# Performance work log

Measured on AMD Instinct MI355X. Metric: run time of the kernel, lower is better.

The kernel has to match this reference:

```python
import jax, jax.numpy as jnp
import numpy as np

T, B, L = 40, 64, 80
D_IN = 256
H = 4 * D_IN  # 1024
A = 18


def _lstm_scan(x, h0, c0, W_ih, W_hh, b_ih, b_hh):
    # x: [S,B,in] -> outputs [S,B,H]; PyTorch gate order i,f,g,o
    b = b_ih + b_hh
    def step(carry, xt):
        h, c = carry
        g = xt @ W_ih.T + h @ W_hh.T + b
        i, f, gg, o = jnp.split(g, 4, axis=-1)
        c = jax.nn.sigmoid(f) * c + jax.nn.sigmoid(i) * jnp.tanh(gg)
        h = jax.nn.sigmoid(o) * jnp.tanh(c)
        return (h, c), h
    (h, c), ys = jax.lax.scan(step, (h0, c0), x)
    return ys, h, c


def setup_inputs() -> dict:
    key = jax.random.key(0)
    ks = jax.random.split(key, 24)
    def rn(k, shape, scale=0.02):
        return jax.random.normal(k, shape, dtype=jnp.float32) * scale
    return {
        "state": rn(ks[0], (T, B, D_IN), 1.0),
        "demonstration": rn(ks[1], (T, B, L, D_IN), 1.0),
        "demonstration_length": jax.random.randint(ks[2], (T, B), 1, L + 1, dtype=jnp.int32),
        "h0": jnp.zeros((B, H), jnp.float32),
        "c0": jnp.zeros((B, H), jnp.float32),
        "enc_Wih": rn(ks[3], (4 * H, D_IN)),
        "enc_Whh": rn(ks[4], (4 * H, H)),
        "enc_bih": rn(ks[5], (4 * H,)),
        "enc_bhh": rn(ks[6], (4 * H,)),
        "attn_W": rn(ks[7], (1, 2 * H)),
        "attn_b": rn(ks[8], (1,)),
        "comb_W": rn(ks[9], (H, H + D_IN)),
        "comb_b": rn(ks[10], (H,)),
        "lstm_Wih": rn(ks[11], (4 * H, H)),
        "lstm_Whh": rn(ks[12], (4 * H, H)),
        "lstm_bih": rn(ks[13], (4 * H,)),
        "lstm_bhh": rn(ks[14], (4 * H,)),
        "mid_W": rn(ks[15], (H, H)),
        "mid_b": rn(ks[16], (H,)),
        "out_W": rn(ks[17], (A, H)),
        "out_b": rn(ks[18], (A,)),
    }


def reference(state, demonstration, demonstration_length, h0, c0,
              enc_Wih, enc_Whh, enc_bih, enc_bhh,
              attn_W, attn_b, comb_W, comb_b,
              lstm_Wih, lstm_Whh, lstm_bih, lstm_bhh,
              mid_W, mid_b, out_W, out_b):
    lengths = demonstration_length[0]              # [B], only t=0 lengths used (as in original)
    demo0 = demonstration[0]                       # [B,L,D_IN], only t=0 demo used
    z = jnp.zeros((B, H), demo0.dtype)
    enc, _, _ = _lstm_scan(demo0.transpose(1, 0, 2), z, z,
                           enc_Wih, enc_Whh, enc_bih, enc_bhh)  # [L,B,H]
    enc = enc.transpose(1, 0, 2)                   # [B,L,H]
    mask = jnp.arange(L)[None, :] < lengths[:, None]  # [B,L]
    # attn(cat(enc, h)) == enc @ Wd^T + h @ Wh^T + b (split of the concat linear)
    Wd, Wh = attn_W[:, :H], attn_W[:, H:]          # [1,H] each
    score_d = (enc @ Wd.T)[..., 0] + attn_b[0]     # [B,L], constant over t
    lstm_b = lstm_bih + lstm_bhh

    def step(carry, obs_t):
        h, c = carry
        scores = score_d + h @ Wh.T                # [B,L] ([B,1] broadcast)
        scores = jnp.where(mask, scores, -jnp.inf)
        w = jax.nn.softmax(scores, axis=-1)        # masked softmax over demo steps
        attn_applied = jnp.einsum('bl,blh->bh', w, enc)
        x = jax.nn.relu(jnp.concatenate([attn_applied, obs_t], axis=-1) @ comb_W.T + comb_b)
        g = x @ lstm_Wih.T + h @ lstm_Whh.T + lstm_b
        i, f, gg, o = jnp.split(g, 4, axis=-1)
        c = jax.nn.sigmoid(f) * c + jax.nn.sigmoid(i) * jnp.tanh(gg)
        h = jax.nn.sigmoid(o) * jnp.tanh(c)
        m = h @ mid_W.T + mid_b                    # no activation between middle and output (as in source)
        q_t = m @ out_W.T + out_b
        return (h, c), q_t

    (h, c), q = jax.lax.scan(step, (h0, c0), state)  # q: [T,B,A]
    return q, h, c
```

## Files before the change

kernel.cpp:

```cpp
#include <hip/hip_runtime.h>
#include <hip/hip_bf16.h>

#define TT 40
#define BB 64
#define LL 80
#define DD 256
#define HH 1024
#define G4H 4096
#define AA 18
#define KENC 1280
#define KLSTM 2048
#define KCOMB 1280
#define NB 256
#define NT 512
#define QSZ (TT*BB*AA)

typedef __bf16 bf16x8 __attribute__((ext_vector_type(8)));
typedef float  f32x4  __attribute__((ext_vector_type(4)));

#define OFF_WENC   ((size_t)0)
#define OFF_WLSTM  (OFF_WENC  + (size_t)G4H*KENC*2)
#define OFF_WCOMB  (OFF_WLSTM + (size_t)G4H*KLSTM*2)
#define OFF_WMID   (OFF_WCOMB + (size_t)HH*KCOMB*2)
#define OFF_BIASE  (OFF_WMID  + (size_t)HH*HH*2)
#define OFF_BIASL  (OFF_BIASE + (size_t)G4H*4)
#define OFF_DEMO   (OFF_BIASL + (size_t)G4H*4)
#define OFF_STATE  (OFF_DEMO  + (size_t)BB*LL*DD*2)
#define OFF_ENC    (OFF_STATE + (size_t)TT*BB*DD*2)
#define OFF_HDEC   (OFF_ENC   + (size_t)BB*LL*HH*2)
#define OFF_XALL   (OFF_HDEC  + (size_t)TT*BB*HH*2)
#define OFF_MF     (OFF_XALL  + (size_t)TT*BB*HH*2)
#define OFF_ATTNS  (OFF_MF    + (size_t)TT*BB*HH*2)
#define OFF_HROT   (OFF_ATTNS + (size_t)BB*HH*2)
#define NSLOT_E    81
#define NSLOT_D    41
#define OFF_BAR    (OFF_HROT  + (size_t)(NSLOT_E+NSLOT_D)*BB*HH*2)
#define FLAG_STRIDE 16
#define BAR_BYTES  (NB*FLAG_STRIDE*4)

__device__ __forceinline__ float sigm(float x){ return 1.f/(1.f+__expf(-x)); }

__device__ __forceinline__ float wred_sum(float v){
#pragma unroll
  for (int s=32; s>0; s>>=1) v += __shfl_xor(v, s, 64);
  return v;
}
__device__ __forceinline__ float wred_max(float v){
#pragma unroll
  for (int s=32; s>0; s>>=1) v = fmaxf(v, __shfl_xor(v, s, 64));
  return v;
}

__device__ __forceinline__ unsigned pack_bf16(float a, float b){
  unsigned short ua = __builtin_bit_cast(unsigned short, (__bf16)a);
  unsigned short ub = __builtin_bit_cast(unsigned short, (__bf16)b);
  return (unsigned)ua | ((unsigned)ub << 16);
}

__device__ __forceinline__ void st_u32_sc(unsigned* p, unsigned v){
  __hip_atomic_store(p, v, __ATOMIC_RELAXED, __HIP_MEMORY_SCOPE_AGENT);
}
__device__ __forceinline__ void st_b16_sc(__bf16* p, float v){
  unsigned short u = __builtin_bit_cast(unsigned short, (__bf16)v);
  asm volatile("global_store_short %0, %1, off sc0 sc1"
               :: "v"(p), "v"((unsigned)u) : "memory");
}

__device__ __forceinline__ void gbar_arrive(unsigned* flags, unsigned target, int bk){
  __syncthreads();
  if (threadIdx.x == 0) {
    __builtin_amdgcn_fence(__ATOMIC_RELEASE, "agent");
    __hip_atomic_store(flags + (size_t)bk*FLAG_STRIDE, target,
                       __ATOMIC_RELAXED, __HIP_MEMORY_SCOPE_AGENT);
  }
}
__device__ __forceinline__ void gbar_wait(unsigned* flags, unsigned target){
  if (threadIdx.x < 64) {
    unsigned long long spins = 0;
    for (;;) {
      unsigned a0 = __hip_atomic_load(flags + (size_t)threadIdx.x*FLAG_STRIDE,       __ATOMIC_RELAXED, __HIP_MEMORY_SCOPE_AGENT);
      unsigned a1 = __hip_atomic_load(flags + (size_t)(64+threadIdx.x)*FLAG_STRIDE,  __ATOMIC_RELAXED, __HIP_MEMORY_SCOPE_AGENT);
      unsigned a2 = __hip_atomic_load(flags + (size_t)(128+threadIdx.x)*FLAG_STRIDE, __ATOMIC_RELAXED, __HIP_MEMORY_SCOPE_AGENT);
      unsigned a3 = __hip_atomic_load(flags + (size_t)(192+threadIdx.x)*FLAG_STRIDE, __ATOMIC_RELAXED, __HIP_MEMORY_SCOPE_AGENT);
      bool ok = (a0 >= target) && (a1 >= target) && (a2 >= target) && (a3 >= target);
      if (__all((int)ok)) break;
      if (++spins > (1ull<<20)) break;
      __builtin_amdgcn_s_sleep(1);
    }
  }
  __syncthreads();
  asm volatile("" ::: "memory");
}

__global__ void k_pack_enc(const float* __restrict__ wih, const float* __restrict__ whh,
                           const float* __restrict__ bih, const float* __restrict__ bhh,
                           __bf16* __restrict__ dst, float* __restrict__ bias){
  int p = blockIdx.x;
  int gate = p & 3, jj = (p >> 2) & 3, bq = p >> 4;
  int orig = gate*HH + bq*4 + jj;
  if (threadIdx.x == 0) bias[p] = bih[orig] + bhh[orig];
  const float* s0 = wih + (size_t)orig*DD;
  const float* s1 = whh + (size_t)orig*HH;
  __bf16* d = dst + (size_t)p*KENC;
  for (int k = threadIdx.x; k < KENC; k += blockDim.x)
    d[k] = (__bf16)(k < DD ? s0[k] : s1[k-DD]);
}
__global__ void k_pack_lstm(const float* __restrict__ wih, const float* __restrict__ whh,
                            const float* __restrict__ bih, const float* __restrict__ bhh,
                            __bf16* __restrict__ dst, float* __restrict__ bias){
  int p = blockIdx.x;
  int gate = p & 3, jj = (p >> 2) & 3, bq = p >> 4;
  int orig = gate*HH + bq*4 + jj;
  if (threadIdx.x == 0) bias[p] = bih[orig] + bhh[orig];
  const float* s0 = wih + (size_t)orig*HH;
  const float* s1 = whh + (size_t)orig*HH;
  __bf16* d = dst + (size_t)p*KLSTM;
  for (int k = threadIdx.x; k < KLSTM; k += blockDim.x)
    d[k] = (__bf16)(k < HH ? s0[k] : s1[k-HH]);
}
__global__ void k_conv(const float* __restrict__ src, __bf16* __restrict__ dst, int n){
  int i = blockIdx.x*blockDim.x + threadIdx.x;
  if (i < n) dst[i] = (__bf16)src[i];
}

__global__ __launch_bounds__(NT, 1)
void k_main(const int* __restrict__ demlen,
            const float* __restrict__ h0, const float* __restrict__ c0,
            const float* __restrict__ attn_w,
            const float* __restrict__ comb_b, const float* __restrict__ mid_b,
            const float* __restrict__ out_w, const float* __restrict__ out_b,
            float* __restrict__ out, char* __restrict__ ws){
  const int bk = blockIdx.x, tid = threadIdx.x;
  const int wv = tid >> 6, ln = tid & 63;
  const int l15 = ln & 15, lhi = ln >> 4;
  const int klane = lhi * 8;
  const int gtid = bk*NT + tid;

  __bf16* wEnc  = (__bf16*)(ws + OFF_WENC);
  __bf16* wLstm = (__bf16*)(ws + OFF_WLSTM);
  __bf16* wComb = (__bf16*)(ws + OFF_WCOMB);
  __bf16* wMid  = (__bf16*)(ws + OFF_WMID);
  const float* bE = (const float*)(ws + OFF_BIASE);
  const float* bL = (const float*)(ws + OFF_BIASL);
  __bf16* demoC = (__bf16*)(ws + OFF_DEMO);
  __bf16* stateB= (__bf16*)(ws + OFF_STATE);
  __bf16* encB  = (__bf16*)(ws + OFF_ENC);
  __bf16* hdec  = (__bf16*)(ws + OFF_HDEC);
  __bf16* xall  = (__bf16*)(ws + OFF_XALL);
  __bf16* mf    = (__bf16*)(ws + OFF_MF);
  __bf16* attnS = (__bf16*)(ws + OFF_ATTNS);
  __bf16* hrotE = (__bf16*)(ws + OFF_HROT);
  __bf16* hrotD = hrotE + (size_t)NSLOT_E*BB*HH;
  unsigned* flags = (unsigned*)(ws + OFF_BAR);

  __shared__ float g_lds [BB*17];
  __shared__ float g_lds2[BB*17];
  __shared__ float sc_sh[LL];
  __shared__ float w_sh[LL];

  unsigned bar = 0;
  const int m_ = tid >> 1, q2 = tid & 1;
  const int j0_ = bk*4 + 2*q2;
  const int mt = wv & 3;
  const int am = mt*16 + l15;
  const int khalf = wv >> 2;

  float cfa = 0.f, cfb = 0.f;

  for (int i = gtid; i < BB*HH/2; i += NB*NT) st_u32_sc((unsigned*)hrotE + i, 0u);
  ++bar; gbar_arrive(flags, bar, bk);

  for (int t = 0; t < LL; ++t) {
    gbar_wait(flags, bar);
    const __bf16* hR = hrotE + (size_t)t*BB*HH;
    const __bf16* brow = wEnc + (size_t)(bk*16 + l15)*KENC;
    const int kbase = khalf * 640;

    f32x4 acc = {0.f,0.f,0.f,0.f};
#pragma unroll 8
    for (int kk = 0; kk < 640; kk += 32) {
      int k0 = kbase + kk + klane;
      const __bf16* pa = (k0 < DD) ? demoC + ((size_t)am*LL + t)*DD + k0
                                   : hR + (size_t)am*HH + (k0 - DD);
      acc = __builtin_amdgcn_mfma_f32_16x16x32_bf16(*(const bf16x8*)pa,
                                                    *(const bf16x8*)(brow + k0), acc, 0,0,0);
    }
    {
      float* gl = khalf ? g_lds2 : g_lds;
      int r0 = mt*16 + lhi*4;
#pragma unroll
      for (int r = 0; r < 4; ++r) gl[(r0+r)*17 + l15] = acc[r];
    }
    __syncthreads();
    if (tid < 128) {
      char* hWg = (char*)(hrotE + (size_t)(t+1)*BB*HH);
      int gb = m_*17 + q2*8, cb = bk*16 + q2*8;
      float gi0 = g_lds[gb+0]+g_lds2[gb+0]+bE[cb+0], gf0 = g_lds[gb+1]+g_lds2[gb+1]+bE[cb+1];
      float gg0 = g_lds[gb+2]+g_lds2[gb+2]+bE[cb+2], go0 = g_lds[gb+3]+g_lds2[gb+3]+bE[cb+3];
      float gi1 = g_lds[gb+4]+g_lds2[gb+4]+bE[cb+4], gf1 = g_lds[gb+5]+g_lds2[gb+5]+bE[cb+5];
      float gg1 = g_lds[gb+6]+g_lds2[gb+6]+bE[cb+6], go1 = g_lds[gb+7]+g_lds2[gb+7]+bE[cb+7];
      float cn0 = sigm(gf0)*cfa + sigm(gi0)*tanhf(gg0);
      float cn1 = sigm(gf1)*cfb + sigm(gi1)*tanhf(gg1);
      float hn0 = sigm(go0)*tanhf(cn0);
      float hn1 = sigm(go1)*tanhf(cn1);
      cfa = cn0; cfb = cn1;
      unsigned hp = pack_bf16(hn0, hn1);
      st_u32_sc((unsigned*)(hWg + m_*2048 + j0_*2), hp);
      st_u32_sc((unsigned*)(encB + ((size_t)m_*LL + t)*HH + j0_), hp);
    }
    ++bar; gbar_arrive(flags, bar, bk);
  }

  gbar_wait(flags, bar);
  {
    int b = bk >> 2, qq = bk & 3;
    for (int i = 0; i < 10; ++i) {
      int l = wv*10 + i;
      const __bf16* er = encB + ((size_t)b*LL + l)*HH + ln*16;
      bf16x8 e0 = *(const bf16x8*)(er);
      bf16x8 e1 = *(const bf16x8*)(er + 8);
      float part = 0.f;
#pragma unroll
      for (int j = 0; j < 8; ++j) {
        part += (float)e0[j] * attn_w[ln*16 + j];
        part += (float)e1[j] * attn_w[ln*16 + 8 + j];
      }
      part = wred_sum(part);
      if (ln == 0) sc_sh[l] = part;
    }
    __syncthreads();
    if (wv == 0) {
      int len = demlen[b];
      float s0 = (ln < len) ? sc_sh[ln] : -1e30f;
      float s1 = (ln < 16 && 64+ln < len) ? sc_sh[64+ln] : -1e30f;
      float mx = wred_max(fmaxf(s0, s1));
      float e0 = __expf(s0 - mx);
      float e1 = (ln < 16) ? __expf(s1 - mx) : 0.f;
      float inv = 1.f / wred_sum(e0 + e1);
      w_sh[ln] = e0 * inv;
      if (ln < 16) w_sh[64+ln] = e1 * inv;
    }
    __syncthreads();
    if (tid < 256) {
      int col = qq*256 + tid;
      float a = 0.f;
      const __bf16* eb = encB + (size_t)b*LL*HH + col;
#pragma unroll 4
      for (int l = 0; l < LL; ++l) a += w_sh[l] * (float)eb[(size_t)l*HH];
      st_b16_sc(attnS + (size_t)b*HH + col, a);
    }
    for (int i = gtid; i < BB*HH/2; i += NB*NT) {
      int i2 = i*2;
      st_u32_sc((unsigned*)hrotD + i, pack_bf16(h0[i2], h0[i2+1]));
    }
    if (tid < 128) {
      cfa = c0[m_*HH + j0_];
      cfb = c0[m_*HH + j0_ + 1];
    }
  }
  ++bar; gbar_arrive(flags, bar, bk);

  gbar_wait(flags, bar);
  {
    int g = bk*8 + wv;
    for (int i = 0; i < 5; ++i) {
      int ti = i*2048 + g;
      int mtt = ti >> 6, nt = ti & 63;
      f32x4 acc = {0.f,0.f,0.f,0.f};
      const __bf16* brow = wComb + (size_t)(nt*16 + l15)*KCOMB;
      int r = mtt*16 + l15, bb = r & 63;
      const __bf16* aat = attnS + (size_t)bb*HH;
      const __bf16* ast = stateB + (size_t)r*DD;
#pragma unroll 8
      for (int kk = 0; kk < KCOMB; kk += 32) {
        int k0 = kk + klane;
        bf16x8 af = (k0 < HH) ? *(const bf16x8*)(aat + k0)
                              : *(const bf16x8*)(ast + (k0-HH));
        acc = __builtin_amdgcn_mfma_f32_16x16x32_bf16(af, *(const bf16x8*)(brow + k0), acc, 0,0,0);
      }
      int col = nt*16 + l15;
      float cb = comb_b[col];
      int r0 = mtt*16 + lhi*4;
#pragma unroll
      for (int rr = 0; rr < 4; ++rr)
        st_b16_sc(xall + (size_t)(r0+rr)*HH + col, fmaxf(acc[rr]+cb, 0.f));
    }
  }
  ++bar; gbar_arrive(flags, bar, bk);

  for (int t = 0; t < TT; ++t) {
    gbar_wait(flags, bar);
    const __bf16* hR = hrotD + (size_t)t*BB*HH;
    const __bf16* brow = wLstm + (size_t)(bk*16 + l15)*KLSTM;
    const int kbase = khalf * HH;
    const __bf16* arow = khalf ? (hR + (size_t)am*HH)
                               : (xall + ((size_t)t*BB + am)*HH);

    f32x4 acc = {0.f,0.f,0.f,0.f};
#pragma unroll 8
    for (int kk = 0; kk < HH; kk += 32) {
      int k0 = kk + klane;
      acc = __builtin_amdgcn_mfma_f32_16x16x32_bf16(*(const bf16x8*)(arow + k0),
                                                    *(const bf16x8*)(brow + kbase + k0), acc, 0,0,0);
    }
    {
      float* gl = khalf ? g_lds2 : g_lds;
      int r0 = mt*16 + lhi*4;
#pragma unroll
      for (int r = 0; r < 4; ++r) gl[(r0+r)*17 + l15] = acc[r];
    }
    __syncthreads();
    if (tid < 128) {
      char* hWg = (char*)(hrotD + (size_t)(t+1)*BB*HH);
      int gb = m_*17 + q2*8, cb = bk*16 + q2*8;
      float gi0 = g_lds[gb+0]+g_lds2[gb+0]+bL[cb+0], gf0 = g_lds[gb+1]+g_lds2[gb+1]+bL[cb+1];
      float gg0 = g_lds[gb+2]+g_lds2[gb+2]+bL[cb+2], go0 = g_lds[gb+3]+g_lds2[gb+3]+bL[cb+3];
      float gi1 = g_lds[gb+4]+g_lds2[gb+4]+bL[cb+4], gf1 = g_lds[gb+5]+g_lds2[gb+5]+bL[cb+5];
      float gg1 = g_lds[gb+6]+g_lds2[gb+6]+bL[cb+6], go1 = g_lds[gb+7]+g_lds2[gb+7]+bL[cb+7];
      float cn0 = sigm(gf0)*cfa + sigm(gi0)*tanhf(gg0);
      float cn1 = sigm(gf1)*cfb + sigm(gi1)*tanhf(gg1);
      float hn0 = sigm(go0)*tanhf(cn0);
      float hn1 = sigm(go1)*tanhf(cn1);
      cfa = cn0; cfb = cn1;
      unsigned hp = pack_bf16(hn0, hn1);
      st_u32_sc((unsigned*)(hWg + m_*2048 + j0_*2), hp);
      st_u32_sc((unsigned*)(hdec + ((size_t)t*BB + m_)*HH + j0_), hp);
      if (t == TT-1) {
        out[QSZ + m_*HH + j0_]     = hn0;
        out[QSZ + m_*HH + j0_ + 1] = hn1;
      }
    }
    ++bar; gbar_arrive(flags, bar, bk);
  }

  if (tid < 128) {
    out[QSZ + BB*HH + m_*HH + j0_]     = cfa;
    out[QSZ + BB*HH + m_*HH + j0_ + 1] = cfb;
  }

  gbar_wait(flags, bar);
  {
    int g = bk*8 + wv;
    for (int i = 0; i < 5; ++i) {
      int ti = i*2048 + g;
      int mtt = ti >> 6, nt = ti & 63;
      f32x4 acc = {0.f,0.f,0.f,0.f};
      const __bf16* brow = wMid + (size_t)(nt*16 + l15)*HH;
      const __bf16* arow2 = hdec + (size_t)(mtt*16 + l15)*HH;
#pragma unroll 8
      for (int kk = 0; kk < HH; kk += 32) {
        int k0 = kk + klane;
        acc = __builtin_amdgcn_mfma_f32_16x16x32_bf16(*(const bf16x8*)(arow2 + k0),
                                                      *(const bf16x8*)(brow + k0), acc, 0,0,0);
      }
      int col = nt*16 + l15;
      float mb = mid_b[col];
      int r0 = mtt*16 + lhi*4;
#pragma unroll
      for (int rr = 0; rr < 4; ++rr)
        st_b16_sc(mf + (size_t)(r0+rr)*HH + col, acc[rr]+mb);
    }
  }
  ++bar; gbar_arrive(flags, bar, bk);

  gbar_wait(flags, bar);
  {
    int g = bk*8 + wv;
    for (int i = 0; i < 2; ++i) {
      int row = i*2048 + g;
      if (row < TT*BB) {
        const __bf16* mr = mf + (size_t)row*HH;
        float mreg[16];
#pragma unroll
        for (int k = 0; k < 16; ++k) mreg[k] = (float)mr[ln + 64*k];
        for (int a = 0; a < AA; ++a) {
          float p = 0.f;
#pragma unroll
          for (int k = 0; k < 16; ++k) p += mreg[k] * out_w[(size_t)a*HH + ln + 64*k];
          p = wred_sum(p);
          if (ln == 0) out[(size_t)row*AA + a] = p + out_b[a];
        }
      }
    }
  }
}

extern "C" void kernel_launch(void* const* d_in, const int* in_sizes, int n_in,
                              void* d_out, int out_size, void* d_ws, size_t ws_size,
                              hipStream_t stream) {
  (void)in_sizes; (void)n_in; (void)out_size; (void)ws_size;
  const float* state    = (const float*)d_in[0];
  const float* demo     = (const float*)d_in[1];
  const int*   demlen   = (const int*)d_in[2];
  const float* h0       = (const float*)d_in[3];
  const float* c0       = (const float*)d_in[4];
  const float* enc_wih  = (const float*)d_in[5];
  const float* enc_whh  = (const float*)d_in[6];
  const float* enc_bih  = (const float*)d_in[7];
  const float* enc_bhh  = (const float*)d_in[8];
  const float* attn_w   = (const float*)d_in[9];
  const float* comb_w   = (const float*)d_in[11];
  const float* comb_b   = (const float*)d_in[12];
  const float* lstm_wih = (const float*)d_in[13];
  const float* lstm_whh = (const float*)d_in[14];
  const float* lstm_bih = (const float*)d_in[15];
  const float* lstm_bhh = (const float*)d_in[16];
  const float* mid_w    = (const float*)d_in[17];
  const float* mid_b    = (const float*)d_in[18];
  const float* out_w    = (const float*)d_in[19];
  const float* out_b    = (const float*)d_in[20];
  char* ws = (char*)d_ws;

  (void)hipMemsetAsync(ws + OFF_BAR, 0, BAR_BYTES, stream);
  k_pack_enc <<<G4H, 256, 0, stream>>>(enc_wih, enc_whh, enc_bih, enc_bhh,
                                       (__bf16*)(ws + OFF_WENC), (float*)(ws + OFF_BIASE));
  k_pack_lstm<<<G4H, 256, 0, stream>>>(lstm_wih, lstm_whh, lstm_bih, lstm_bhh,
                                       (__bf16*)(ws + OFF_WLSTM), (float*)(ws + OFF_BIASL));
  k_conv<<<(HH*KCOMB + 255)/256, 256, 0, stream>>>(comb_w, (__bf16*)(ws + OFF_WCOMB), HH*KCOMB);
  k_conv<<<(HH*HH   + 255)/256, 256, 0, stream>>>(mid_w,  (__bf16*)(ws + OFF_WMID),  HH*HH);
  k_conv<<<(BB*LL*DD + 255)/256, 256, 0, stream>>>(demo,  (__bf16*)(ws + OFF_DEMO),  BB*LL*DD);
  k_conv<<<(TT*BB*DD + 255)/256, 256, 0, stream>>>(state, (__bf16*)(ws + OFF_STATE), TT*BB*DD);
  k_main<<<NB, NT, 0, stream>>>(demlen, h0, c0, attn_w, comb_b, mid_b,
                                out_w, out_b, (float*)d_out, ws);
}
```

Before: 2.125 ms.

## Replace persistent grid-barrier kernel with per-timestep kernel launches

Splits the single persistent kernel, which synchronised 256 blocks through spin-wait flag barriers, into separate launches: one per encoder step, one per decoder step, plus attention, combine, mid and output kernels. The h state ping-pongs between two buffers and the cell state lives in a global buffer instead of registers. This removes the cost of the software grid barrier and its sc0/sc1 coherent stores, but adds about 125 kernel launches with their launch latency and gaps.

```diff
diff --git a/kernel.cpp b/kernel.cpp
--- a/kernel.cpp
+++ b/kernel.cpp
@@ -11,8 +11,6 @@
 #define KENC 1280
 #define KLSTM 2048
 #define KCOMB 1280
-#define NB 256
-#define NT 512
 #define QSZ (TT*BB*AA)
 
 typedef __bf16 bf16x8 __attribute__((ext_vector_type(8)));
@@ -31,12 +29,8 @@
 #define OFF_XALL   (OFF_HDEC  + (size_t)TT*BB*HH*2)
 #define OFF_MF     (OFF_XALL  + (size_t)TT*BB*HH*2)
 #define OFF_ATTNS  (OFF_MF    + (size_t)TT*BB*HH*2)
-#define OFF_HROT   (OFF_ATTNS + (size_t)BB*HH*2)
-#define NSLOT_E    81
-#define NSLOT_D    41
-#define OFF_BAR    (OFF_HROT  + (size_t)(NSLOT_E+NSLOT_D)*BB*HH*2)
-#define FLAG_STRIDE 16
-#define BAR_BYTES  (NB*FLAG_STRIDE*4)
+#define OFF_CF     (OFF_ATTNS + (size_t)BB*HH*2)
+#define OFF_HBUF   (OFF_CF    + (size_t)BB*HH*4)
 
 __device__ __forceinline__ float sigm(float x){ return 1.f/(1.f+__expf(-x)); }
 
@@ -50,46 +44,10 @@
   for (int s=32; s>0; s>>=1) v = fmaxf(v, __shfl_xor(v, s, 64));
   return v;
 }
-
 __device__ __forceinline__ unsigned pack_bf16(float a, float b){
   unsigned short ua = __builtin_bit_cast(unsigned short, (__bf16)a);
   unsigned short ub = __builtin_bit_cast(unsigned short, (__bf16)b);
   return (unsigned)ua | ((unsigned)ub << 16);
-}
-
-__device__ __forceinline__ void st_u32_sc(unsigned* p, unsigned v){
-  __hip_atomic_store(p, v, __ATOMIC_RELAXED, __HIP_MEMORY_SCOPE_AGENT);
-}
-__device__ __forceinline__ void st_b16_sc(__bf16* p, float v){
-  unsigned short u = __builtin_bit_cast(unsigned short, (__bf16)v);
-  asm volatile("global_store_short %0, %1, off sc0 sc1"
-               :: "v"(p), "v"((unsigned)u) : "memory");
-}
-
-__device__ __forceinline__ void gbar_arrive(unsigned* flags, unsigned target, int bk){
-  __syncthreads();
-  if (threadIdx.x == 0) {
-    __builtin_amdgcn_fence(__ATOMIC_RELEASE, "agent");
-    __hip_atomic_store(flags + (size_t)bk*FLAG_STRIDE, target,
-                       __ATOMIC_RELAXED, __HIP_MEMORY_SCOPE_AGENT);
-  }
-}
-__device__ __forceinline__ void gbar_wait(unsigned* flags, unsigned target){
-  if (threadIdx.x < 64) {
-    unsigned long long spins = 0;
-    for (;;) {
-      unsigned a0 = __hip_atomic_load(flags + (size_t)threadIdx.x*FLAG_STRIDE,       __ATOMIC_RELAXED, __HIP_MEMORY_SCOPE_AGENT);
-      unsigned a1 = __hip_atomic_load(flags + (size_t)(64+threadIdx.x)*FLAG_STRIDE,  __ATOMIC_RELAXED, __HIP_MEMORY_SCOPE_AGENT);
-      unsigned a2 = __hip_atomic_load(flags + (size_t)(128+threadIdx.x)*FLAG_STRIDE, __ATOMIC_RELAXED, __HIP_MEMORY_SCOPE_AGENT);
-      unsigned a3 = __hip_atomic_load(flags + (size_t)(192+threadIdx.x)*FLAG_STRIDE, __ATOMIC_RELAXED, __HIP_MEMORY_SCOPE_AGENT);
-      bool ok = (a0 >= target) && (a1 >= target) && (a2 >= target) && (a3 >= target);
-      if (__all((int)ok)) break;
-      if (++spins > (1ull<<20)) break;
-      __builtin_amdgcn_s_sleep(1);
-    }
-  }
-  __syncthreads();
-  asm volatile("" ::: "memory");
 }
 
 __global__ void k_pack_enc(const float* __restrict__ wih, const float* __restrict__ whh,
@@ -123,266 +81,257 @@
   if (i < n) dst[i] = (__bf16)src[i];
 }
 
-__global__ __launch_bounds__(NT, 1)
-void k_main(const int* __restrict__ demlen,
-            const float* __restrict__ h0, const float* __restrict__ c0,
-            const float* __restrict__ attn_w,
-            const float* __restrict__ comb_b, const float* __restrict__ mid_b,
-            const float* __restrict__ out_w, const float* __restrict__ out_b,
-            float* __restrict__ out, char* __restrict__ ws){
+__global__ __launch_bounds__(256)
+void k_enc_step(const __bf16* __restrict__ demoC, const __bf16* __restrict__ wEnc,
+                const float* __restrict__ bE, const __bf16* __restrict__ hR,
+                __bf16* __restrict__ hW, __bf16* __restrict__ encB,
+                float* __restrict__ cf, int t){
   const int bk = blockIdx.x, tid = threadIdx.x;
   const int wv = tid >> 6, ln = tid & 63;
   const int l15 = ln & 15, lhi = ln >> 4;
   const int klane = lhi * 8;
-  const int gtid = bk*NT + tid;
-
-  __bf16* wEnc  = (__bf16*)(ws + OFF_WENC);
-  __bf16* wLstm = (__bf16*)(ws + OFF_WLSTM);
-  __bf16* wComb = (__bf16*)(ws + OFF_WCOMB);
-  __bf16* wMid  = (__bf16*)(ws + OFF_WMID);
-  const float* bE = (const float*)(ws + OFF_BIASE);
-  const float* bL = (const float*)(ws + OFF_BIASL);
-  __bf16* demoC = (__bf16*)(ws + OFF_DEMO);
-  __bf16* stateB= (__bf16*)(ws + OFF_STATE);
-  __bf16* encB  = (__bf16*)(ws + OFF_ENC);
-  __bf16* hdec  = (__bf16*)(ws + OFF_HDEC);
-  __bf16* xall  = (__bf16*)(ws + OFF_XALL);
-  __bf16* mf    = (__bf16*)(ws + OFF_MF);
-  __bf16* attnS = (__bf16*)(ws + OFF_ATTNS);
-  __bf16* hrotE = (__bf16*)(ws + OFF_HROT);
-  __bf16* hrotD = hrotE + (size_t)NSLOT_E*BB*HH;
-  unsigned* flags = (unsigned*)(ws + OFF_BAR);
-
-  __shared__ float g_lds [BB*17];
-  __shared__ float g_lds2[BB*17];
-  __shared__ float sc_sh[LL];
-  __shared__ float w_sh[LL];
-
-  unsigned bar = 0;
-  const int m_ = tid >> 1, q2 = tid & 1;
-  const int j0_ = bk*4 + 2*q2;
+  const int am = wv*16 + l15;
+
+  __shared__ float g_lds[BB*17];
+
+  const __bf16* brow = wEnc + (size_t)(bk*16 + l15)*KENC;
+  const __bf16* arow = demoC + ((size_t)am*LL + t)*DD;
+  const __bf16* hrow = hR + (size_t)am*HH;
+
+  f32x4 acc = {0.f,0.f,0.f,0.f};
+#pragma unroll 8
+  for (int kk = 0; kk < KENC; kk += 32) {
+    int k0 = kk + klane;
+    const __bf16* pa = (k0 < DD) ? (arow + k0) : (hrow + (k0 - DD));
+    acc = __builtin_amdgcn_mfma_f32_16x16x32_bf16(*(const bf16x8*)pa,
+                                                  *(const bf16x8*)(brow + k0), acc, 0,0,0);
+  }
+  {
+    int r0 = wv*16 + lhi*4;
+#pragma unroll
+    for (int r = 0; r < 4; ++r) g_lds[(r0+r)*17 + l15] = acc[r];
+  }
+  __syncthreads();
+  if (tid < 128) {
+    const int m_ = tid >> 1, q2 = tid & 1;
+    const int j0_ = bk*4 + 2*q2;
+    int gb = m_*17 + q2*8, cb = bk*16 + q2*8;
+    float gi0 = g_lds[gb+0]+bE[cb+0], gf0 = g_lds[gb+1]+bE[cb+1];
+    float gg0 = g_lds[gb+2]+bE[cb+2], go0 = g_lds[gb+3]+bE[cb+3];
+    float gi1 = g_lds[gb+4]+bE[cb+4], gf1 = g_lds[gb+5]+bE[cb+5];
+    float gg1 = g_lds[gb+6]+bE[cb+6], go1 = g_lds[gb+7]+bE[cb+7];
+    float cA = cf[m_*HH + j0_], cB = cf[m_*HH + j0_ + 1];
+    float cn0 = sigm(gf0)*cA + sigm(gi0)*tanhf(gg0);
+    float cn1 = sigm(gf1)*cB + sigm(gi1)*tanhf(gg1);
+    float hn0 = sigm(go0)*tanhf(cn0);
+    float hn1 = sigm(go1)*tanhf(cn1);
+    cf[m_*HH + j0_] = cn0; cf[m_*HH + j0_ + 1] = cn1;
+    unsigned hp = pack_bf16(hn0, hn1);
+    *(unsigned*)(hW + (size_t)m_*HH + j0_) = hp;
+    *(unsigned*)(encB + ((size_t)m_*LL + t)*HH + j0_) = hp;
+  }
+}
+
+__global__ __launch_bounds__(512)
+void k_dec_step(const __bf16* __restrict__ xall, const __bf16* __restrict__ wLstm,
+                const float* __restrict__ bL, const __bf16* __restrict__ hR,
+                __bf16* __restrict__ hW, __bf16* __restrict__ hdec,
+                float* __restrict__ cf, float* __restrict__ out, int t){
+  const int bk = blockIdx.x, tid = threadIdx.x;
+  const int wv = tid >> 6, ln = tid & 63;
+  const int l15 = ln & 15, lhi = ln >> 4;
+  const int klane = lhi * 8;
   const int mt = wv & 3;
   const int am = mt*16 + l15;
   const int khalf = wv >> 2;
 
-  float cfa = 0.f, cfb = 0.f;
-
-  for (int i = gtid; i < BB*HH/2; i += NB*NT) st_u32_sc((unsigned*)hrotE + i, 0u);
-  ++bar; gbar_arrive(flags, bar, bk);
-
-  for (int t = 0; t < LL; ++t) {
-    gbar_wait(flags, bar);
-    const __bf16* hR = hrotE + (size_t)t*BB*HH;
-    const __bf16* brow = wEnc + (size_t)(bk*16 + l15)*KENC;
-    const int kbase = khalf * 640;
-
+  __shared__ float g_lds [BB*17];
+  __shared__ float g_lds2[BB*17];
+
+  const __bf16* brow = wLstm + (size_t)(bk*16 + l15)*KLSTM + khalf*HH;
+  const __bf16* arow = khalf ? (hR + (size_t)am*HH)
+                             : (xall + ((size_t)t*BB + am)*HH);
+
+  f32x4 acc = {0.f,0.f,0.f,0.f};
+#pragma unroll 8
+  for (int kk = 0; kk < HH; kk += 32) {
+    int k0 = kk + klane;
+    acc = __builtin_amdgcn_mfma_f32_16x16x32_bf16(*(const bf16x8*)(arow + k0),
+                                                  *(const bf16x8*)(brow + k0), acc, 0,0,0);
+  }
+  {
+    float* gl = khalf ? g_lds2 : g_lds;
+    int r0 = mt*16 + lhi*4;
+#pragma unroll
+    for (int r = 0; r < 4; ++r) gl[(r0+r)*17 + l15] = acc[r];
+  }
+  __syncthreads();
+  if (tid < 128) {
+    const int m_ = tid >> 1, q2 = tid & 1;
+    const int j0_ = bk*4 + 2*q2;
+    int gb = m_*17 + q2*8, cb = bk*16 + q2*8;
+    float gi0 = g_lds[gb+0]+g_lds2[gb+0]+bL[cb+0], gf0 = g_lds[gb+1]+g_lds2[gb+1]+bL[cb+1];
+    float gg0 = g_lds[gb+2]+g_lds2[gb+2]+bL[cb+2], go0 = g_lds[gb+3]+g_lds2[gb+3]+bL[cb+3];
+    float gi1 = g_lds[gb+4]+g_lds2[gb+4]+bL[cb+4], gf1 = g_lds[gb+5]+g_lds2[gb+5]+bL[cb+5];
+    float gg1 = g_lds[gb+6]+g_lds2[gb+6]+bL[cb+6], go1 = g_lds[gb+7]+g_lds2[gb+7]+bL[cb+7];
+    float cA = cf[m_*HH + j0_], cB = cf[m_*HH + j0_ + 1];
+    float cn0 = sigm(gf0)*cA + sigm(gi0)*tanhf(gg0);
+    float cn1 = sigm(gf1)*cB + sigm(gi1)*tanhf(gg1);
+    float hn0 = sigm(go0)*tanhf(cn0);
+    float hn1 = sigm(go1)*tanhf(cn1);
+    cf[m_*HH + j0_] = cn0; cf[m_*HH + j0_ + 1] = cn1;
+    unsigned hp = pack_bf16(hn0, hn1);
+    *(unsigned*)(hW + (size_t)m_*HH + j0_) = hp;
+    *(unsigned*)(hdec + ((size_t)t*BB + m_)*HH + j0_) = hp;
+    if (t == TT-1) {
+      out[QSZ + m_*HH + j0_]     = hn0;
+      out[QSZ + m_*HH + j0_ + 1] = hn1;
+    }
+  }
+}
+
+__global__ __launch_bounds__(256)
+void k_attn(const int* __restrict__ demlen, const float* __restrict__ h0,
+            const float* __restrict__ c0, const float* __restrict__ attn_w,
+            const __bf16* __restrict__ encB, __bf16* __restrict__ attnS,
+            __bf16* __restrict__ hD0, float* __restrict__ cf){
+  const int bk = blockIdx.x, tid = threadIdx.x;
+  const int wv = tid >> 6, ln = tid & 63;
+  __shared__ float sc_sh[LL];
+  __shared__ float w_sh[LL];
+  int b = bk >> 2, qq = bk & 3;
+  for (int i = 0; i < 20; ++i) {
+    int l = wv*20 + i;
+    const __bf16* er = encB + ((size_t)b*LL + l)*HH + ln*16;
+    bf16x8 e0 = *(const bf16x8*)(er);
+    bf16x8 e1 = *(const bf16x8*)(er + 8);
+    float part = 0.f;
+#pragma unroll
+    for (int j = 0; j < 8; ++j) {
+      part += (float)e0[j] * attn_w[ln*16 + j];
+      part += (float)e1[j] * attn_w[ln*16 + 8 + j];
+    }
+    part = wred_sum(part);
+    if (ln == 0) sc_sh[l] = part;
+  }
+  __syncthreads();
+  if (wv == 0) {
+    int len = demlen[b];
+    float s0 = (ln < len) ? sc_sh[ln] : -1e30f;
+    float s1 = (ln < 16 && 64+ln < len) ? sc_sh[64+ln] : -1e30f;
+    float mx = wred_max(fmaxf(s0, s1));
+    float e0 = __expf(s0 - mx);
+    float e1 = (ln < 16) ? __expf(s1 - mx) : 0.f;
+    float inv = 1.f / wred_sum(e0 + e1);
+    w_sh[ln] = e0 * inv;
+    if (ln < 16) w_sh[64+ln] = e1 * inv;
+  }
+  __syncthreads();
+  {
+    int col = qq*256 + tid;
+    float a = 0.f;
+    const __bf16* eb = encB + (size_t)b*LL*HH + col;
+#pragma unroll 4
+    for (int l = 0; l < LL; ++l) a += w_sh[l] * (float)eb[(size_t)l*HH];
+    attnS[(size_t)b*HH + col] = (__bf16)a;
+  }
+  int gtid = bk*256 + tid;
+  for (int i = gtid; i < BB*HH/2; i += 256*256) {
+    int i2 = i*2;
+    *((unsigned*)hD0 + i) = pack_bf16(h0[i2], h0[i2+1]);
+  }
+  for (int i = gtid; i < BB*HH; i += 256*256) cf[i] = c0[i];
+}
+
+__global__ __launch_bounds__(256)
+void k_x(const __bf16* __restrict__ attnS, const __bf16* __restrict__ stateB,
+         const __bf16* __restrict__ wComb, const float* __restrict__ comb_b,
+         __bf16* __restrict__ xall){
+  const int bk = blockIdx.x, tid = threadIdx.x;
+  const int wv = tid >> 6, ln = tid & 63;
+  const int l15 = ln & 15, lhi = ln >> 4;
+  const int klane = lhi * 8;
+  int g = bk*4 + wv;
+  for (int i = 0; i < 10; ++i) {
+    int ti = i*1024 + g;
+    int mtt = ti >> 6, nt = ti & 63;
     f32x4 acc = {0.f,0.f,0.f,0.f};
+    const __bf16* brow = wComb + (size_t)(nt*16 + l15)*KCOMB;
+    int r = mtt*16 + l15, bb = r & 63;
+    const __bf16* aat = attnS + (size_t)bb*HH;
+    const __bf16* ast = stateB + (size_t)r*DD;
 #pragma unroll 8
-    for (int kk = 0; kk < 640; kk += 32) {
-      int k0 = kbase + kk + klane;
-      const __bf16* pa = (k0 < DD) ? demoC + ((size_t)am*LL + t)*DD + k0
-                                   : hR + (size_t)am*HH + (k0 - DD);
-      acc = __builtin_amdgcn_mfma_f32_16x16x32_bf16(*(const bf16x8*)pa,
-                                                    *(const bf16x8*)(brow + k0), acc, 0,0,0);
+    for (int kk = 0; kk < KCOMB; kk += 32) {
+      int k0 = kk + klane;
+      bf16x8 af = (k0 < HH) ? *(const bf16x8*)(aat + k0)
+                            : *(const bf16x8*)(ast + (k0-HH));
+      acc = __builtin_amdgcn_mfma_f32_16x16x32_bf16(af, *(const bf16x8*)(brow + k0), acc, 0,0,0);
     }
-    {
-      float* gl = khalf ? g_lds2 : g_lds;
-      int r0 = mt*16 + lhi*4;
-#pragma unroll
-      for (int r = 0; r < 4; ++r) gl[(r0+r)*17 + l15] = acc[r];
-    }
-    __syncthreads();
-    if (tid < 128) {
-      char* hWg = (char*)(hrotE + (size_t)(t+1)*BB*HH);
-      int gb = m_*17 + q2*8, cb = bk*16 + q2*8;
-      float gi0 = g_lds[gb+0]+g_lds2[gb+0]+bE[cb+0], gf0 = g_lds[gb+1]+g_lds2[gb+1]+bE[cb+1];
-      float gg0 = g_lds[gb+2]+g_lds2[gb+2]+bE[cb+2], go0 = g_lds[gb+3]+g_lds2[gb+3]+bE[cb+3];
-      float gi1 = g_lds[gb+4]+g_lds2[gb+4]+bE[cb+4], gf1 = g_lds[gb+5]+g_lds2[gb+5]+bE[cb+5];
-      float gg1 = g_lds[gb+6]+g_lds2[gb+6]+bE[cb+6], go1 = g_lds[gb+7]+g_lds2[gb+7]+bE[cb+7];
-      float cn0 = sigm(gf0)*cfa + sigm(gi0)*tanhf(gg0);
-      float cn1 = sigm(gf1)*cfb + sigm(gi1)*tanhf(gg1);
-      float hn0 = sigm(go0)*tanhf(cn0);
-      float hn1 = sigm(go1)*tanhf(cn1);
-      cfa = cn0; cfb = cn1;
-      unsigned hp = pack_bf16(hn0, hn1);
-      st_u32_sc((unsigned*)(hWg + m_*2048 + j0_*2), hp);
-      st_u32_sc((unsigned*)(encB + ((size_t)m_*LL + t)*HH + j0_), hp);
-    }
-    ++bar; gbar_arrive(flags, bar, bk);
-  }
-
-  gbar_wait(flags, bar);
-  {
-    int b = bk >> 2, qq = bk & 3;
-    for (int i = 0; i < 10; ++i) {
-      int l = wv*10 + i;
-      const __bf16* er = encB + ((size_t)b*LL + l)*HH + ln*16;
-      bf16x8 e0 = *(const bf16x8*)(er);
-      bf16x8 e1 = *(const bf16x8*)(er + 8);
-      float part = 0.f;
-#pragma unroll
-      for (int j = 0; j < 8; ++j) {
-        part += (float)e0[j] * attn_w[ln*16 + j];
-        part += (float)e1[j] * attn_w[ln*16 + 8 + j];
-      }
-      part = wred_sum(part);
-      if (ln == 0) sc_sh[l] = part;
-    }
-    __syncthreads();
-    if (wv == 0) {
-      int len = demlen[b];
-      float s0 = (ln < len) ? sc_sh[ln] : -1e30f;
-      float s1 = (ln < 16 && 64+ln < len) ? sc_sh[64+ln] : -1e30f;
-      float mx = wred_max(fmaxf(s0, s1));
-      float e0 = __expf(s0 - mx);
-      float e1 = (ln < 16) ? __expf(s1 - mx) : 0.f;
-      float inv = 1.f / wred_sum(e0 + e1);
-      w_sh[ln] = e0 * inv;
-      if (ln < 16) w_sh[64+ln] = e1 * inv;
-    }
-    __syncthreads();
-    if (tid < 256) {
-      int col = qq*256 + tid;
-      float a = 0.f;
-      const __bf16* eb = encB + (size_t)b*LL*HH + col;
-#pragma unroll 4
-      for (int l = 0; l < LL; ++l) a += w_sh[l] * (float)eb[(size_t)l*HH];
-      st_b16_sc(attnS + (size_t)b*HH + col, a);
-    }
-    for (int i = gtid; i < BB*HH/2; i += NB*NT) {
-      int i2 = i*2;
-      st_u32_sc((unsigned*)hrotD + i, pack_bf16(h0[i2], h0[i2+1]));
-    }
-    if (tid < 128) {
-      cfa = c0[m_*HH + j0_];
-      cfb = c0[m_*HH + j0_ + 1];
-    }
-  }
-  ++bar; gbar_arrive(flags, bar, bk);
-
-  gbar_wait(flags, bar);
-  {
-    int g = bk*8 + wv;
-    for (int i = 0; i < 5; ++i) {
-      int ti = i*2048 + g;
-      int mtt = ti >> 6, nt = ti & 63;
-      f32x4 acc = {0.f,0.f,0.f,0.f};
-      const __bf16* brow = wComb + (size_t)(nt*16 + l15)*KCOMB;
-      int r = mtt*16 + l15, bb = r & 63;
-      const __bf16* aat = attnS + (size_t)bb*HH;
-      const __bf16* ast = stateB + (size_t)r*DD;
-#pragma unroll 8
-      for (int kk = 0; kk < KCOMB; kk += 32) {
-        int k0 = kk + klane;
-        bf16x8 af = (k0 < HH) ? *(const bf16x8*)(aat + k0)
-                              : *(const bf16x8*)(ast + (k0-HH));
-        acc = __builtin_amdgcn_mfma_f32_16x16x32_bf16(af, *(const bf16x8*)(brow + k0), acc, 0,0,0);
-      }
-      int col = nt*16 + l15;
-      float cb = comb_b[col];
-      int r0 = mtt*16 + lhi*4;
-#pragma unroll
-      for (int rr = 0; rr < 4; ++rr)
-        st_b16_sc(xall + (size_t)(r0+rr)*HH + col, fmaxf(acc[rr]+cb, 0.f));
-    }
-  }
-  ++bar; gbar_arrive(flags, bar, bk);
-
-  for (int t = 0; t < TT; ++t) {
-    gbar_wait(flags, bar);
-    const __bf16* hR = hrotD + (size_t)t*BB*HH;
-    const __bf16* brow = wLstm + (size_t)(bk*16 + l15)*KLSTM;
-    const int kbase = khalf * HH;
-    const __bf16* arow = khalf ? (hR + (size_t)am*HH)
-                               : (xall + ((size_t)t*BB + am)*HH);
-
+    int col = nt*16 + l15;
+    float cb = comb_b[col];
+    int r0 = mtt*16 + lhi*4;
+#pragma unroll
+    for (int rr = 0; rr < 4; ++rr)
+      xall[(size_t)(r0+rr)*HH + col] = (__bf16)fmaxf(acc[rr]+cb, 0.f);
+  }
+}
+
+__global__ __launch_bounds__(256)
+void k_mid(const __bf16* __restrict__ hdec, const __bf16* __restrict__ wMid,
+           const float* __restrict__ mid_b, __bf16* __restrict__ mf){
+  const int bk = blockIdx.x, tid = threadIdx.x;
+  const int wv = tid >> 6, ln = tid & 63;
+  const int l15 = ln & 15, lhi = ln >> 4;
+  const int klane = lhi * 8;
+  int g = bk*4 + wv;
+  for (int i = 0; i < 10; ++i) {
+    int ti = i*1024 + g;
+    int mtt = ti >> 6, nt = ti & 63;
     f32x4 acc = {0.f,0.f,0.f,0.f};
+    const __bf16* brow = wMid + (size_t)(nt*16 + l15)*HH;
+    const __bf16* arow = hdec + (size_t)(mtt*16 + l15)*HH;
 #pragma unroll 8
     for (int kk = 0; kk < HH; kk += 32) {
       int k0 = kk + klane;
       acc = __builtin_amdgcn_mfma_f32_16x16x32_bf16(*(const bf16x8*)(arow + k0),
-                                                    *(const bf16x8*)(brow + kbase + k0), acc, 0,0,0);
+                                                    *(const bf16x8*)(brow + k0), acc, 0,0,0);
     }
-    {
-      float* gl = khalf ? g_lds2 : g_lds;
-      int r0 = mt*16 + lhi*4;
-#pragma unroll
-      for (int r = 0; r < 4; ++r) gl[(r0+r)*17 + l15] = acc[r];
-    }
-    __syncthreads();
-    if (tid < 128) {
-      char* hWg = (char*)(hrotD + (size_t)(t+1)*BB*HH);
-      int gb = m_*17 + q2*8, cb = bk*16 + q2*8;
-      float gi0 = g_lds[gb+0]+g_lds2[gb+0]+bL[cb+0], gf0 = g_lds[gb+1]+g_lds2[gb+1]+bL[cb+1];
-      float gg0 = g_lds[gb+2]+g_lds2[gb+2]+bL[cb+2], go0 = g_lds[gb+3]+g_lds2[gb+3]+bL[cb+3];
-      float gi1 = g_lds[gb+4]+g_lds2[gb+4]+bL[cb+4], gf1 = g_lds[gb+5]+g_lds2[gb+5]+bL[cb+5];
-      float gg1 = g_lds[gb+6]+g_lds2[gb+6]+bL[cb+6], go1 = g_lds[gb+7]+g_lds2[gb+7]+bL[cb+7];
-      float cn0 = sigm(gf0)*cfa + sigm(gi0)*tanhf(gg0);
-      float cn1 = sigm(gf1)*cfb + sigm(gi1)*tanhf(gg1);
-      float hn0 = sigm(go0)*tanhf(cn0);
-      float hn1 = sigm(go1)*tanhf(cn1);
-      cfa = cn0; cfb = cn1;
-      unsigned hp = pack_bf16(hn0, hn1);
-      st_u32_sc((unsigned*)(hWg + m_*2048 + j0_*2), hp);
-      st_u32_sc((unsigned*)(hdec + ((size_t)t*BB + m_)*HH + j0_), hp);
-      if (t == TT-1) {
-        out[QSZ + m_*HH + j0_]     = hn0;
-        out[QSZ + m_*HH + j0_ + 1] = hn1;
+    int col = nt*16 + l15;
+    float mb = mid_b[col];
+    int r0 = mtt*16 + lhi*4;
+#pragma unroll
+    for (int rr = 0; rr < 4; ++rr)
+      mf[(size_t)(r0+rr)*HH + col] = (__bf16)(acc[rr]+mb);
+  }
+}
+
+__global__ __launch_bounds__(256)
+void k_out(const __bf16* __restrict__ mf, const float* __restrict__ out_w,
+           const float* __restrict__ out_b, float* __restrict__ out){
+  const int bk = blockIdx.x, tid = threadIdx.x;
+  const int wv = tid >> 6, ln = tid & 63;
+  int g = bk*4 + wv;
+  for (int i = 0; i < 3; ++i) {
+    int row = i*1024 + g;
+    if (row < TT*BB) {
+      const __bf16* mr = mf + (size_t)row*HH;
+      float mreg[16];
+#pragma unroll
+      for (int k = 0; k < 16; ++k) mreg[k] = (float)mr[ln + 64*k];
+      for (int a = 0; a < AA; ++a) {
+        float p = 0.f;
+#pragma unroll
+        for (int k = 0; k < 16; ++k) p += mreg[k] * out_w[(size_t)a*HH + ln + 64*k];
+        p = wred_sum(p);
+        if (ln == 0) out[(size_t)row*AA + a] = p + out_b[a];
       }
     }
-    ++bar; gbar_arrive(flags, bar, bk);
-  }
-
-  if (tid < 128) {
-    out[QSZ + BB*HH + m_*HH + j0_]     = cfa;
-    out[QSZ + BB*HH + m_*HH + j0_ + 1] = cfb;
-  }
-
-  gbar_wait(flags, bar);
-  {
-    int g = bk*8 + wv;
-    for (int i = 0; i < 5; ++i) {
-      int ti = i*2048 + g;
-      int mtt = ti >> 6, nt = ti & 63;
-      f32x4 acc = {0.f,0.f,0.f,0.f};
-      const __bf16* brow = wMid + (size_t)(nt*16 + l15)*HH;
-      const __bf16* arow2 = hdec + (size_t)(mtt*16 + l15)*HH;
-#pragma unroll 8
-      for (int kk = 0; kk < HH; kk += 32) {
-        int k0 = kk + klane;
-        acc = __builtin_amdgcn_mfma_f32_16x16x32_bf16(*(const bf16x8*)(arow2 + k0),
-                                                      *(const bf16x8*)(brow + k0), acc, 0,0,0);
-      }
-      int col = nt*16 + l15;
-      float mb = mid_b[col];
-      int r0 = mtt*16 + lhi*4;
-#pragma unroll
-      for (int rr = 0; rr < 4; ++rr)
-        st_b16_sc(mf + (size_t)(r0+rr)*HH + col, acc[rr]+mb);
-    }
-  }
-  ++bar; gbar_arrive(flags, bar, bk);
-
-  gbar_wait(flags, bar);
-  {
-    int g = bk*8 + wv;
-    for (int i = 0; i < 2; ++i) {
-      int row = i*2048 + g;
-      if (row < TT*BB) {
-        const __bf16* mr = mf + (size_t)row*HH;
-        float mreg[16];
-#pragma unroll
-        for (int k = 0; k < 16; ++k) mreg[k] = (float)mr[ln + 64*k];
-        for (int a = 0; a < AA; ++a) {
-          float p = 0.f;
-#pragma unroll
-          for (int k = 0; k < 16; ++k) p += mreg[k] * out_w[(size_t)a*HH + ln + 64*k];
-          p = wred_sum(p);
-          if (ln == 0) out[(size_t)row*AA + a] = p + out_b[a];
-        }
-      }
-    }
-  }
+  }
+}
+
+__global__ void k_fin(const float* __restrict__ cf, float* __restrict__ out){
+  int i = blockIdx.x*blockDim.x + threadIdx.x;
+  if (i < BB*HH) out[QSZ + BB*HH + i] = cf[i];
 }
 
 extern "C" void kernel_launch(void* const* d_in, const int* in_sizes, int n_in,
@@ -411,15 +360,48 @@
   const float* out_b    = (const float*)d_in[20];
   char* ws = (char*)d_ws;
 
-  (void)hipMemsetAsync(ws + OFF_BAR, 0, BAR_BYTES, stream);
-  k_pack_enc <<<G4H, 256, 0, stream>>>(enc_wih, enc_whh, enc_bih, enc_bhh,
-                                       (__bf16*)(ws + OFF_WENC), (float*)(ws + OFF_BIASE));
-  k_pack_lstm<<<G4H, 256, 0, stream>>>(lstm_wih, lstm_whh, lstm_bih, lstm_bhh,
-                                       (__bf16*)(ws + OFF_WLSTM), (float*)(ws + OFF_BIASL));
-  k_conv<<<(HH*KCOMB + 255)/256, 256, 0, stream>>>(comb_w, (__bf16*)(ws + OFF_WCOMB), HH*KCOMB);
-  k_conv<<<(HH*HH   + 255)/256, 256, 0, stream>>>(mid_w,  (__bf16*)(ws + OFF_WMID),  HH*HH);
-  k_conv<<<(BB*LL*DD + 255)/256, 256, 0, stream>>>(demo,  (__bf16*)(ws + OFF_DEMO),  BB*LL*DD);
-  k_conv<<<(TT*BB*DD + 255)/256, 256, 0, stream>>>(state, (__bf16*)(ws + OFF_STATE), TT*BB*DD);
-  k_main<<<NB, NT, 0, stream>>>(demlen, h0, c0, attn_w, comb_b, mid_b,
-                                out_w, out_b, (float*)d_out, ws);
-}
+  __bf16* wEnc  = (__bf16*)(ws + OFF_WENC);
+  __bf16* wLstm = (__bf16*)(ws + OFF_WLSTM);
+  __bf16* wComb = (__bf16*)(ws + OFF_WCOMB);
+  __bf16* wMid  = (__bf16*)(ws + OFF_WMID);
+  float*  bE    = (float*)(ws + OFF_BIASE);
+  float*  bL    = (float*)(ws + OFF_BIASL);
+  __bf16* demoC = (__bf16*)(ws + OFF_DEMO);
+  __bf16* stateB= (__bf16*)(ws + OFF_STATE);
+  __bf16* encB  = (__bf16*)(ws + OFF_ENC);
+  __bf16* hdec  = (__bf16*)(ws + OFF_HDEC);
+  __bf16* xall  = (__bf16*)(ws + OFF_XALL);
+  __bf16* mf    = (__bf16*)(ws + OFF_MF);
+  __bf16* attnS = (__bf16*)(ws + OFF_ATTNS);
+  float*  cf    = (float*)(ws + OFF_CF);
+  __bf16* hbE0  = (__bf16*)(ws + OFF_HBUF);
+  __bf16* hbE1  = hbE0 + (size_t)BB*HH;
+  __bf16* hbD0  = hbE1 + (size_t)BB*HH;
+  __bf16* hbD1  = hbD0 + (size_t)BB*HH;
+  float*  out   = (float*)d_out;
+
+  (void)hipMemsetAsync(cf,   0, (size_t)BB*HH*4, stream);
+  (void)hipMemsetAsync(hbE0, 0, (size_t)BB*HH*2, stream);
+  k_pack_enc <<<G4H, 256, 0, stream>>>(enc_wih, enc_whh, enc_bih, enc_bhh, wEnc, bE);
+  k_pack_lstm<<<G4H, 256, 0, stream>>>(lstm_wih, lstm_whh, lstm_bih, lstm_bhh, wLstm, bL);
+  k_conv<<<(HH*KCOMB + 255)/256, 256, 0, stream>>>(comb_w, wComb, HH*KCOMB);
+  k_conv<<<(HH*HH   + 255)/256, 256, 0, stream>>>(mid_w,  wMid,  HH*HH);
+  k_conv<<<(BB*LL*DD + 255)/256, 256, 0, stream>>>(demo,  demoC,  BB*LL*DD);
+  k_conv<<<(TT*BB*DD + 255)/256, 256, 0, stream>>>(state, stateB, TT*BB*DD);
+
+  for (int t = 0; t < LL; ++t) {
+    __bf16* hR = (t & 1) ? hbE1 : hbE0;
+    __bf16* hW = (t & 1) ? hbE0 : hbE1;
+    k_enc_step<<<256, 256, 0, stream>>>(demoC, wEnc, bE, hR, hW, encB, cf, t);
+  }
+  k_attn<<<256, 256, 0, stream>>>(demlen, h0, c0, attn_w, encB, attnS, hbD0, cf);
+  k_x<<<256, 256, 0, stream>>>(attnS, stateB, wComb, comb_b, xall);
+  for (int t = 0; t < TT; ++t) {
+    __bf16* hR = (t & 1) ? hbD1 : hbD0;
+    __bf16* hW = (t & 1) ? hbD0 : hbD1;
+    k_dec_step<<<256, 512, 0, stream>>>(xall, wLstm, bL, hR, hW, hdec, cf, out, t);
+  }
+  k_mid<<<256, 256, 0, stream>>>(hdec, wMid, mid_b, mf);
+  k_out<<<256, 256, 0, stream>>>(mf, out_w, out_b, out);
+  k_fin<<<(BB*HH + 255)/256, 256, 0, stream>>>(cf, out);
+}
```

New measurement: 1.915 ms. 9.9% less time.
